# Kernel optimization log

Measured on AMD Instinct MI355X. Metric: run time of the kernel, lower is better.

The kernel has to match this reference:

```python
import jax, jax.numpy as jnp
import numpy as np

H = 3584          # hidden_size
NH = 28           # num query heads
NKV = 4           # num kv heads
HD = H // NH      # head_dim = 128
I = 18944         # intermediate_size
EPS = 1e-6
THETA = 1000000.0


def setup_inputs() -> dict:
    key = jax.random.key(0)
    ks = jax.random.split(key, 16)
    B, S = 1, 2048
    s = 0.02
    inp = {
        "hidden_states": jax.random.normal(ks[0], (B, S, H), jnp.float32),
        "position_ids": jnp.broadcast_to(jnp.arange(S, dtype=jnp.int32)[None, :], (B, S)),
        "q_w": jax.random.normal(ks[1], (NH * HD, H), jnp.float32) * s,
        "q_b": jax.random.normal(ks[2], (NH * HD,), jnp.float32) * s,
        "k_w": jax.random.normal(ks[3], (NKV * HD, H), jnp.float32) * s,
        "k_b": jax.random.normal(ks[4], (NKV * HD,), jnp.float32) * s,
        "v_w": jax.random.normal(ks[5], (NKV * HD, H), jnp.float32) * s,
        "v_b": jax.random.normal(ks[6], (NKV * HD,), jnp.float32) * s,
        "o_w": jax.random.normal(ks[7], (H, NH * HD), jnp.float32) * s,
        "gate_w": jax.random.normal(ks[8], (I, H), jnp.float32) * s,
        "up_w": jax.random.normal(ks[9], (I, H), jnp.float32) * s,
        "down_w": jax.random.normal(ks[10], (H, I), jnp.float32) * s,
        "ln1_w": jnp.ones((H,), jnp.float32),
        "ln2_w": jnp.ones((H,), jnp.float32),
    }
    return inp


def _rms_norm(x, w):
    var = jnp.mean(jnp.square(x), axis=-1, keepdims=True)
    return x * jax.lax.rsqrt(var + EPS) * w


def _rope_cos_sin(position_ids):
    # inv_freq: [HD/2]
    inv_freq = 1.0 / (THETA ** (jnp.arange(0, HD, 2, dtype=jnp.float32) / HD))
    ang = position_ids.astype(jnp.float32)[..., None] * inv_freq  # [B,S,HD/2]
    emb = jnp.concatenate([ang, ang], axis=-1)                     # [B,S,HD]
    return jnp.cos(emb)[:, None], jnp.sin(emb)[:, None]            # [B,1,S,HD]


def _rotate_half(x):
    x1, x2 = x[..., : HD // 2], x[..., HD // 2 :]
    return jnp.concatenate([-x2, x1], axis=-1)


def _forward(hidden_states, position_ids, q_w, q_b, k_w, k_b, v_w, v_b,
             o_w, gate_w, up_w, down_w, ln1_w, ln2_w):
    B, S, _ = hidden_states.shape
    residual = hidden_states
    x = _rms_norm(hidden_states, ln1_w)

    q = jnp.einsum("bsh,dh->bsd", x, q_w) + q_b   # [B,S,NH*HD]
    k = jnp.einsum("bsh,dh->bsd", x, k_w) + k_b   # [B,S,NKV*HD]
    v = jnp.einsum("bsh,dh->bsd", x, v_w) + v_b

    q = q.reshape(B, S, NH, HD).transpose(0, 2, 1, 3)    # [B,NH,S,HD]
    k = k.reshape(B, S, NKV, HD).transpose(0, 2, 1, 3)   # [B,NKV,S,HD]
    v = v.reshape(B, S, NKV, HD).transpose(0, 2, 1, 3)

    cos, sin = _rope_cos_sin(position_ids)
    q = q * cos + _rotate_half(q) * sin
    k = k * cos + _rotate_half(k) * sin

    # GQA: group query heads per kv head (NH = NKV * G)
    G = NH // NKV
    qg = q.reshape(B, NKV, G, S, HD)
    scores = jnp.einsum("bhgsd,bhtd->bhgst", qg, k) / jnp.sqrt(jnp.float32(HD))
    probs = jax.nn.softmax(scores, axis=-1)               # no causal mask in source
    attn = jnp.einsum("bhgst,bhtd->bhgsd", probs, v)      # [B,NKV,G,S,HD]
    attn = attn.reshape(B, NH, S, HD).transpose(0, 2, 1, 3).reshape(B, S, H)

    attn_out = jnp.einsum("bsd,hd->bsh", attn, o_w)
    hidden = residual + attn_out

    residual = hidden
    x = _rms_norm(hidden, ln2_w)
    gate = jax.nn.silu(jnp.einsum("bsh,ih->bsi", x, gate_w))
    up = jnp.einsum("bsh,ih->bsi", x, up_w)
    mlp = jnp.einsum("bsi,hi->bsh", gate * up, down_w)
    return residual + mlp


def reference(hidden_states, position_ids, q_w, q_b, k_w, k_b, v_w, v_b,
              o_w, gate_w, up_w, down_w, ln1_w, ln2_w):
    return _forward(hidden_states, position_ids, q_w, q_b, k_w, k_b, v_w, v_b,
                    o_w, gate_w, up_w, down_w, ln1_w, ln2_w)
```

## Files before the change

### kernel.cpp

```cpp
#include <hip/hip_runtime.h>
#include <hip/hip_bf16.h>
#include <stdint.h>

#define S_LEN 2048
#define HDIM  3584
#define NHEAD 28
#define NKVH  4
#define HDHD  128
#define IDIM  18944

typedef __attribute__((ext_vector_type(8))) short short8;
typedef __attribute__((ext_vector_type(4))) float floatx4;
typedef __attribute__((ext_vector_type(4))) unsigned int uint4v;

__device__ __forceinline__ unsigned short f2bf(float f) {
  union { float f; unsigned int u; } v; v.f = f;
  unsigned int r = v.u + 0x7fffu + ((v.u >> 16) & 1u);
  return (unsigned short)(r >> 16);
}
__device__ __forceinline__ float bf2f(unsigned short h) {
  union { unsigned int u; float f; } v; v.u = ((unsigned int)h) << 16;
  return v.f;
}
__device__ __forceinline__ unsigned int pk2(float a, float b) {
  __hip_bfloat162 h = __float22bfloat162_rn(make_float2(a, b));
  union { __hip_bfloat162 h; unsigned int u; } c; c.h = h; return c.u;
}

__device__ __forceinline__ void gload_lds16(const void* g, void* l) {
  __builtin_amdgcn_global_load_lds(
      (const __attribute__((address_space(1))) void*)g,
      (__attribute__((address_space(3))) void*)l, 16, 0, 0);
}

__device__ __forceinline__ int xcd_remap(int id, int total) {
  return (id & 7) * (total >> 3) + (id >> 3);
}

template<int BM, int MODE, bool BIAS>
__global__ __launch_bounds__(512, 2)
void gemm_db(const unsigned short* __restrict__ A, int lda,
             const unsigned short* __restrict__ W,
             const float* __restrict__ bias,
             void* __restrict__ outp, int ldo, int col0,
             const void* __restrict__ aux, int K)
{
  constexpr int MREP = BM / 32;
  constexpr int MSH  = (BM == 256) ? 3 : 4;
  constexpr int MT   = 2048 / BM;
  constexpr int APASS = BM / 64;

  const int g  = xcd_remap(blockIdx.x, gridDim.x);
  const int mb = g & (MT - 1);
  const int nb = g >> MSH;
  const int t  = threadIdx.x;
  const int w  = t >> 6, l = t & 63, lg = l >> 4, lc = l & 15;
  const int wr = w >> 2, wc = w & 3;

  __shared__ __align__(16) unsigned short As[2][BM * 64];
  __shared__ __align__(16) unsigned short Bs[2][256 * 64];

  floatx4 acc[MREP][4] = {};

  const char* Ablk = (const char*)(A + (size_t)mb * BM * lda);
  const char* Wblk = (const char*)(W + (size_t)nb * 256 * K);

  const int trow  = t >> 3;
  const int s_scb = (((t & 7) ^ ((t >> 3) & 7)) << 4);
  const int r_sw  = (lc & 7) << 4;

  const size_t abytes = (size_t)lda * 2;
  const size_t wbytes = (size_t)K * 2;

  auto stage = [&](int buf, int kt) {
    const char* asrc = Ablk + (size_t)kt * 128 + s_scb;
    #pragma unroll
    for (int i = 0; i < APASS; ++i)
      gload_lds16(asrc + (size_t)(i * 64 + trow) * abytes,
                  (char*)As[buf] + i * 8192 + t * 16);
    const char* wsrc = Wblk + (size_t)kt * 128 + s_scb;
    #pragma unroll
    for (int i = 0; i < 4; ++i)
      gload_lds16(wsrc + (size_t)(i * 64 + trow) * wbytes,
                  (char*)Bs[buf] + i * 8192 + t * 16);
  };

  const int nk = K >> 6;
  stage(0, 0);
  __syncthreads();

  int cur = 0;
  for (int kt = 0; kt < nk; ++kt) {
    if (kt + 1 < nk) stage(cur ^ 1, kt + 1);

    const char* ac = (const char*)As[cur];
    const char* bc = (const char*)Bs[cur];
    __builtin_amdgcn_s_setprio(1);
    #pragma unroll
    for (int kk = 0; kk < 2; ++kk) {
      const int ko = kk * 64 + lg * 16;
      short8 bfrag[4];
      #pragma unroll
      for (int n = 0; n < 4; ++n)
        bfrag[n] = *(const short8*)(bc + (wc*64 + n*16 + lc) * 128 + (ko ^ r_sw));
      #pragma unroll
      for (int m = 0; m < MREP; ++m) {
        short8 af = *(const short8*)(ac + (wr*(BM/2) + m*16 + lc) * 128 + (ko ^ r_sw));
        #pragma unroll
        for (int n = 0; n < 4; ++n)
          acc[m][n] = __builtin_amdgcn_mfma_f32_16x16x32_bf16(af, bfrag[n], acc[m][n], 0, 0, 0);
      }
    }
    __builtin_amdgcn_s_setprio(0);
    __syncthreads();
    cur ^= 1;
  }

  float bv[4] = {0.f, 0.f, 0.f, 0.f};
  if (BIAS) {
    #pragma unroll
    for (int n = 0; n < 4; ++n) bv[n] = bias[nb*256 + wc*64 + n*16 + lc];
  }
  #pragma unroll
  for (int m = 0; m < MREP; ++m) {
    #pragma unroll
    for (int n = 0; n < 4; ++n) {
      const int colg = col0 + nb*256 + wc*64 + n*16 + lc;
      #pragma unroll
      for (int j = 0; j < 4; ++j) {
        const int rowg = mb*BM + wr*(BM/2) + m*16 + lg*4 + j;
        const size_t oidx = (size_t)rowg * ldo + colg;
        float v = acc[m][n][j] + bv[n];
        if (MODE == 0) {
          ((float*)outp)[oidx] = v;
        } else if (MODE == 1) {
          ((unsigned short*)outp)[oidx] = f2bf(v);
        } else if (MODE == 2) {
          ((float*)outp)[oidx] = v + ((const float*)aux)[oidx];
        } else {
          float gt = bf2f(((const unsigned short*)aux)[oidx]);
          float sg = gt / (1.f + __expf(-gt));
          ((unsigned short*)outp)[oidx] = f2bf(sg * v);
        }
      }
    }
  }
}

__global__ __launch_bounds__(256)
void cvt_bf16_kernel(const float* __restrict__ in, unsigned short* __restrict__ out, int n8)
{
  int i = blockIdx.x * 256 + threadIdx.x;
  const int stride = gridDim.x * 256;
  for (; i < n8; i += stride) {
    floatx4 a = *(const floatx4*)(in + (size_t)i * 8);
    floatx4 b = *(const floatx4*)(in + (size_t)i * 8 + 4);
    uint4v p;
    p[0] = pk2(a[0], a[1]); p[1] = pk2(a[2], a[3]);
    p[2] = pk2(b[0], b[1]); p[3] = pk2(b[2], b[3]);
    *(uint4v*)(out + (size_t)i * 8) = p;
  }
}

__global__ void pack_bias_kernel(const float* __restrict__ qb, const float* __restrict__ kb,
                                 const float* __restrict__ vb, float* __restrict__ o)
{
  int i = blockIdx.x * 256 + threadIdx.x;
  if (i < 3584) o[i] = qb[i];
  else if (i < 4096) o[i] = kb[i - 3584];
  else if (i < 4608) o[i] = vb[i - 4096];
}

__global__ __launch_bounds__(448)
void rmsnorm_kernel(const float* __restrict__ x, const float* __restrict__ wgt,
                    unsigned short* __restrict__ out)
{
  const int row = blockIdx.x, t = threadIdx.x;
  const float* xp = x + (size_t)row * HDIM + t * 8;
  floatx4 a = *(const floatx4*)xp;
  floatx4 b = *(const floatx4*)(xp + 4);
  float ss = a[0]*a[0]+a[1]*a[1]+a[2]*a[2]+a[3]*a[3]
           + b[0]*b[0]+b[1]*b[1]+b[2]*b[2]+b[3]*b[3];
  #pragma unroll
  for (int mk = 1; mk < 64; mk <<= 1) ss += __shfl_xor(ss, mk, 64);
  __shared__ float wsum[8];
  if ((t & 63) == 0) wsum[t >> 6] = ss;
  __syncthreads();
  float tot = 0.f;
  #pragma unroll
  for (int i = 0; i < 7; ++i) tot += wsum[i];
  const float sc = rsqrtf(tot * (1.f / 3584.f) + 1e-6f);
  const float* wp = wgt + t * 8;
  short8 o;
  #pragma unroll
  for (int e = 0; e < 4; ++e) o[e]   = (short)f2bf(a[e] * sc * wp[e]);
  #pragma unroll
  for (int e = 0; e < 4; ++e) o[4+e] = (short)f2bf(b[e] * sc * wp[4+e]);
  *(short8*)(out + (size_t)row * HDIM + t * 8) = o;
}

__global__ __launch_bounds__(448)
void add_rmsnorm_kernel(const float* __restrict__ x, const float* __restrict__ y,
                        const float* __restrict__ wgt,
                        float* __restrict__ h1, unsigned short* __restrict__ out)
{
  const int row = blockIdx.x, t = threadIdx.x;
  const size_t base = (size_t)row * HDIM + t * 8;
  floatx4 a = *(const floatx4*)(x + base);
  floatx4 b = *(const floatx4*)(x + base + 4);
  floatx4 c = *(const floatx4*)(y + base);
  floatx4 d = *(const floatx4*)(y + base + 4);
  a += c; b += d;
  *(floatx4*)(h1 + base)     = a;
  *(floatx4*)(h1 + base + 4) = b;
  float ss = a[0]*a[0]+a[1]*a[1]+a[2]*a[2]+a[3]*a[3]
           + b[0]*b[0]+b[1]*b[1]+b[2]*b[2]+b[3]*b[3];
  #pragma unroll
  for (int mk = 1; mk < 64; mk <<= 1) ss += __shfl_xor(ss, mk, 64);
  __shared__ float wsum[8];
  if ((t & 63) == 0) wsum[t >> 6] = ss;
  __syncthreads();
  float tot = 0.f;
  #pragma unroll
  for (int i = 0; i < 7; ++i) tot += wsum[i];
  const float sc = rsqrtf(tot * (1.f / 3584.f) + 1e-6f);
  const float* wp = wgt + t * 8;
  short8 o;
  #pragma unroll
  for (int e = 0; e < 4; ++e) o[e]   = (short)f2bf(a[e] * sc * wp[e]);
  #pragma unroll
  for (int e = 0; e < 4; ++e) o[4+e] = (short)f2bf(b[e] * sc * wp[4+e]);
  *(short8*)(out + (size_t)row * HDIM + t * 8) = o;
}

__global__ void rope_table_kernel(const int* __restrict__ pos, float* __restrict__ tab)
{
  int idx = blockIdx.x * 256 + threadIdx.x;
  int s = idx >> 6, d = idx & 63;
  float p = (float)pos[s];
  float inv = expf(-((float)(2 * d) * (1.f / 128.f)) * 13.815510557964274f);
  float ang = p * inv;
  tab[idx] = cosf(ang);
  tab[S_LEN * 64 + idx] = sinf(ang);
}

template<int NHX>
__global__ void rope_apply_kernel(const float* __restrict__ in, const float* __restrict__ tab,
                                  unsigned short* __restrict__ out, int col0)
{
  int idx = blockIdx.x * 256 + threadIdx.x;
  int d = idx & 63;
  int rem = idx >> 6;
  int hh = rem % NHX;
  int s  = rem / NHX;
  const float* ip = in + (size_t)s * 4608 + col0 + hh * HDHD;
  float x1 = ip[d], x2 = ip[64 + d];
  float c  = tab[s * 64 + d];
  float sn = tab[S_LEN * 64 + s * 64 + d];
  unsigned short* op = out + (size_t)s * (NHX * HDHD) + hh * HDHD;
  op[d]      = f2bf(x1 * c - x2 * sn);
  op[64 + d] = f2bf(x2 * c + x1 * sn);
}

__global__ void vtrans_kernel(const float* __restrict__ qkvf, unsigned short* __restrict__ vt)
{
  int idx = blockIdx.x * 256 + threadIdx.x;
  int s = idx & (S_LEN - 1);
  int c = idx >> 11;
  vt[idx] = f2bf(qkvf[(size_t)s * 4608 + 4096 + c]);
}

__global__ __launch_bounds__(256)
void attn_kernel(const unsigned short* __restrict__ Q,
                 const unsigned short* __restrict__ Kr,
                 const unsigned short* __restrict__ Vt,
                 unsigned short* __restrict__ O)
{
  const int g  = xcd_remap(blockIdx.x, gridDim.x);
  const int qb = g & 31;
  const int h  = g >> 5;
  const int kvh = h / 7;
  const int t = threadIdx.x, w = t >> 6, l = t & 63, lg = l >> 4, lc = l & 15;

  __shared__ __align__(16) unsigned short Ks[64 * 128];
  __shared__ __align__(16) unsigned short Vs[128 * 64];
  __shared__ __align__(16) unsigned short Ps[4][16 * 64];

  const int qrow = qb * 64 + w * 16 + lc;
  short8 qf[4];
  {
    const unsigned short* qp = Q + (size_t)qrow * HDIM + h * HDHD + lg * 8;
    #pragma unroll
    for (int kk = 0; kk < 4; ++kk) qf[kk] = *(const short8*)(qp + kk * 32);
  }

  float mrun[4], lrun[4];
  #pragma unroll
  for (int j = 0; j < 4; ++j) { mrun[j] = -1e30f; lrun[j] = 0.f; }
  floatx4 oacc[8] = {};

  const int k_row = t >> 4;
  const int k_scb = (((t & 15) ^ ((t >> 4) & 7)) << 4);
  const int v_row = t >> 3;
  const int v_scb = (((t & 7) ^ ((t >> 3) & 7)) << 4);
  const int r_sw  = (lc & 7) << 4;
  const float scale = 0.08838834764831843f;

  for (int kt = 0; kt < 32; ++kt) {
    #pragma unroll
    for (int i = 0; i < 4; ++i)
      gload_lds16((const char*)Kr + ((size_t)(kt*64 + i*16 + k_row) * 512 + kvh*128) * 2 + k_scb,
                  (char*)Ks + i * 4096 + t * 16);
    #pragma unroll
    for (int i = 0; i < 4; ++i)
      gload_lds16((const char*)Vt + ((size_t)(kvh*128 + i*32 + v_row) * S_LEN) * 2
                      + (size_t)kt * 128 + v_scb,
                  (char*)Vs + i * 4096 + t * 16);
    __syncthreads();

    floatx4 sacc[4] = {};
    #pragma unroll
    for (int kk = 0; kk < 4; ++kk) {
      #pragma unroll
      for (int n = 0; n < 4; ++n) {
        short8 kf = *(const short8*)((const char*)Ks + (n*16 + lc) * 256
                                     + ((kk*64 + lg*16) ^ r_sw));
        sacc[n] = __builtin_amdgcn_mfma_f32_16x16x32_bf16(qf[kk], kf, sacc[n], 0, 0, 0);
      }
    }

    float pv[4][4], mt[4];
    #pragma unroll
    for (int j = 0; j < 4; ++j) {
      float a0 = sacc[0][j]*scale, a1 = sacc[1][j]*scale;
      float a2 = sacc[2][j]*scale, a3 = sacc[3][j]*scale;
      pv[0][j]=a0; pv[1][j]=a1; pv[2][j]=a2; pv[3][j]=a3;
      mt[j] = fmaxf(fmaxf(a0, a1), fmaxf(a2, a3));
    }
    #pragma unroll
    for (int mk = 1; mk < 16; mk <<= 1)
      #pragma unroll
      for (int j = 0; j < 4; ++j)
        mt[j] = fmaxf(mt[j], __shfl_xor(mt[j], mk, 16));

    float corr[4], rs[4];
    #pragma unroll
    for (int j = 0; j < 4; ++j) {
      float mn = fmaxf(mrun[j], mt[j]);
      corr[j] = __expf(mrun[j] - mn);
      mrun[j] = mn;
      rs[j] = 0.f;
    }
    #pragma unroll
    for (int n = 0; n < 4; ++n)
      #pragma unroll
      for (int j = 0; j < 4; ++j) {
        float p = __expf(pv[n][j] - mrun[j]);
        pv[n][j] = p; rs[j] += p;
      }
    #pragma unroll
    for (int mk = 1; mk < 16; mk <<= 1)
      #pragma unroll
      for (int j = 0; j < 4; ++j)
        rs[j] += __shfl_xor(rs[j], mk, 16);
    #pragma unroll
    for (int j = 0; j < 4; ++j) lrun[j] = lrun[j] * corr[j] + rs[j];
    #pragma unroll
    for (int q = 0; q < 8; ++q) {
      oacc[q][0] *= corr[0]; oacc[q][1] *= corr[1];
      oacc[q][2] *= corr[2]; oacc[q][3] *= corr[3];
    }

    char* pw = (char*)Ps[w];
    #pragma unroll
    for (int n = 0; n < 4; ++n)
      #pragma unroll
      for (int j = 0; j < 4; ++j) {
        const int prow = lg*4 + j;
        *(unsigned short*)(pw + prow*128 + ((((n*16 + lc)*2)) ^ ((prow & 7) << 4)))
            = f2bf(pv[n][j]);
      }

    short8 pa[2];
    #pragma unroll
    for (int ks = 0; ks < 2; ++ks)
      pa[ks] = *(const short8*)(pw + lc*128 + ((ks*64 + lg*16) ^ r_sw));
    #pragma unroll
    for (int ks = 0; ks < 2; ++ks)
      #pragma unroll
      for (int q = 0; q < 8; ++q) {
        short8 vf = *(const short8*)((const char*)Vs + (q*16 + lc) * 128
                                     + ((ks*64 + lg*16) ^ r_sw));
        oacc[q] = __builtin_amdgcn_mfma_f32_16x16x32_bf16(pa[ks], vf, oacc[q], 0, 0, 0);
      }
    __syncthreads();
  }

  float invl[4];
  #pragma unroll
  for (int j = 0; j < 4; ++j) invl[j] = 1.f / lrun[j];
  #pragma unroll
  for (int q = 0; q < 8; ++q)
    #pragma unroll
    for (int j = 0; j < 4; ++j) {
      int rowg = qb*64 + w*16 + lg*4 + j;
      int colg = h*HDHD + q*16 + lc;
      O[(size_t)rowg * HDIM + colg] = f2bf(oacc[q][j] * invl[j]);
    }
}

__global__ void sentinel_kernel(float* out, int n) {
  int i = blockIdx.x * 256 + threadIdx.x;
  if (i < n) out[i] = 1.0e6f;
}

extern "C" void kernel_launch(void* const* d_in, const int* in_sizes, int n_in,
                              void* d_out, int out_size, void* d_ws, size_t ws_size,
                              hipStream_t stream)
{
  (void)in_sizes; (void)n_in;
  const float* hidden = (const float*)d_in[0];
  const int*   pos    = (const int*)d_in[1];
  const float* q_w    = (const float*)d_in[2];
  const float* q_b    = (const float*)d_in[3];
  const float* k_w    = (const float*)d_in[4];
  const float* k_b    = (const float*)d_in[5];
  const float* v_w    = (const float*)d_in[6];
  const float* v_b    = (const float*)d_in[7];
  const float* o_w    = (const float*)d_in[8];
  const float* gate_w = (const float*)d_in[9];
  const float* up_w   = (const float*)d_in[10];
  const float* down_w = (const float*)d_in[11];
  const float* ln1    = (const float*)d_in[12];
  const float* ln2    = (const float*)d_in[13];
  float* out = (float*)d_out;
  char* ws = (char*)d_ws;

  unsigned short* XN    = (unsigned short*)(ws + 0);
  float*          QKVF  = (float*)(ws + 14680064);
  unsigned short* QR    = (unsigned short*)(ws + 52428800);
  unsigned short* KR    = (unsigned short*)(ws + 67108864);
  unsigned short* VT    = (unsigned short*)(ws + 69206016);
  float*          ROPET = (float*)(ws + 71303168);
  float*          BQKV  = (float*)(ws + 72351744);
  unsigned short* CTX   = (unsigned short*)(ws + 77594624);
  float*          AO    = (float*)(ws + 92274688);
  unsigned short* GBUF  = (unsigned short*)(ws + 0);
  unsigned short* ACT   = (unsigned short*)(ws + 77594624);
  float*          H1    = (float*)(ws + 155189248);
  unsigned short* XN2   = (unsigned short*)(ws + 184549376);
  unsigned short* WB    = (unsigned short*)(ws + 199229440);
  const size_t NEED_BIG = 199229440 + 135790592;

  if (ws_size < NEED_BIG) {
    sentinel_kernel<<<(out_size + 255) / 256, 256, 0, stream>>>(out, out_size);
    return;
  }

  const int CVG = 2048;

  rope_table_kernel<<<(S_LEN * 64) / 256, 256, 0, stream>>>(pos, ROPET);
  rmsnorm_kernel<<<S_LEN, 448, 0, stream>>>(hidden, ln1, XN);

  pack_bias_kernel<<<18, 256, 0, stream>>>(q_b, k_b, v_b, BQKV);
  cvt_bf16_kernel<<<CVG, 256, 0, stream>>>(q_w, WB,               (3584 * 3584) / 8);
  cvt_bf16_kernel<<<CVG, 256, 0, stream>>>(k_w, WB + 3584 * 3584, (512 * 3584) / 8);
  cvt_bf16_kernel<<<CVG, 256, 0, stream>>>(v_w, WB + 4096 * 3584, (512 * 3584) / 8);

  gemm_db<128, 0, true><<<288, 512, 0, stream>>>(XN, HDIM, WB, BQKV, QKVF, 4608, 0, nullptr, HDIM);

  rope_apply_kernel<28><<<(S_LEN * 28 * 64) / 256, 256, 0, stream>>>(QKVF, ROPET, QR, 0);
  rope_apply_kernel<4><<<(S_LEN * 4 * 64) / 256,  256, 0, stream>>>(QKVF, ROPET, KR, 3584);
  vtrans_kernel<<<(512 * S_LEN) / 256, 256, 0, stream>>>(QKVF, VT);

  cvt_bf16_kernel<<<CVG, 256, 0, stream>>>(o_w, WB, (3584 * 3584) / 8);

  attn_kernel<<<28 * 32, 256, 0, stream>>>(QR, KR, VT, CTX);

  gemm_db<128, 0, false><<<224, 512, 0, stream>>>(CTX, HDIM, WB, nullptr, AO, HDIM, 0, nullptr, HDIM);
  add_rmsnorm_kernel<<<S_LEN, 448, 0, stream>>>(hidden, AO, ln2, H1, XN2);

  cvt_bf16_kernel<<<CVG, 256, 0, stream>>>(gate_w, WB, (IDIM * HDIM) / 8);
  gemm_db<256, 1, false><<<592, 512, 0, stream>>>(XN2, HDIM, WB, nullptr, GBUF, IDIM, 0, nullptr, HDIM);

  cvt_bf16_kernel<<<CVG, 256, 0, stream>>>(up_w, WB, (IDIM * HDIM) / 8);
  gemm_db<256, 3, false><<<592, 512, 0, stream>>>(XN2, HDIM, WB, nullptr, ACT, IDIM, 0, GBUF, HDIM);

  cvt_bf16_kernel<<<CVG, 256, 0, stream>>>(down_w, WB, (HDIM * IDIM) / 8);
  gemm_db<128, 2, false><<<224, 512, 0, stream>>>(ACT, IDIM, WB, nullptr, out, HDIM, 0, H1, IDIM);
}
```

Measured before the change: 1.925 ms.

## Replace syncthreads with vmcnt-gated barriers and use 128-row tiles everywhere

The GEMM main loop now waits only for the previous stage's global-to-LDS loads with s_waitcnt vmcnt(6) and raw s_barrier. This lets the next tile's prefetch stay in flight across the barrier instead of draining all memory ops under __syncthreads. The gate/up GEMMs also switch from 256-row to 128-row M tiles, doubling the grid to 1184 blocks. That gives more parallelism but more weight re-reads and fewer MFMAs per B-fragment load.

```diff
diff --git a/kernel.cpp b/kernel.cpp
--- a/kernel.cpp
+++ b/kernel.cpp
@@ -37,83 +37,87 @@
   return (id & 7) * (total >> 3) + (id >> 3);
 }
 
-template<int BM, int MODE, bool BIAS>
+template<int MODE, bool BIAS>
 __global__ __launch_bounds__(512, 2)
-void gemm_db(const unsigned short* __restrict__ A, int lda,
-             const unsigned short* __restrict__ W,
-             const float* __restrict__ bias,
-             void* __restrict__ outp, int ldo, int col0,
-             const void* __restrict__ aux, int K)
-{
-  constexpr int MREP = BM / 32;
-  constexpr int MSH  = (BM == 256) ? 3 : 4;
-  constexpr int MT   = 2048 / BM;
-  constexpr int APASS = BM / 64;
-
+void gemm_p(const unsigned short* __restrict__ A, int lda,
+            const unsigned short* __restrict__ W,
+            const float* __restrict__ bias,
+            void* __restrict__ outp, int ldo, int col0,
+            const void* __restrict__ aux, int K)
+{
   const int g  = xcd_remap(blockIdx.x, gridDim.x);
-  const int mb = g & (MT - 1);
-  const int nb = g >> MSH;
+  const int mb = g & 15;
+  const int nb = g >> 4;
   const int t  = threadIdx.x;
   const int w  = t >> 6, l = t & 63, lg = l >> 4, lc = l & 15;
   const int wr = w >> 2, wc = w & 3;
 
-  __shared__ __align__(16) unsigned short As[2][BM * 64];
+  __shared__ __align__(16) unsigned short As[2][128 * 64];
   __shared__ __align__(16) unsigned short Bs[2][256 * 64];
 
-  floatx4 acc[MREP][4] = {};
-
-  const char* Ablk = (const char*)(A + (size_t)mb * BM * lda);
+  floatx4 acc[4][4] = {};
+
+  const char* Ablk = (const char*)(A + (size_t)mb * 128 * lda);
   const char* Wblk = (const char*)(W + (size_t)nb * 256 * K);
 
-  const int trow  = t >> 3;
-  const int s_scb = (((t & 7) ^ ((t >> 3) & 7)) << 4);
-  const int r_sw  = (lc & 7) << 4;
+  const int trow = t >> 3;
+  const int scb  = (((t & 7) ^ ((t >> 3) & 7)) << 4);
+  const int r_sw = (lc & 7) << 4;
 
   const size_t abytes = (size_t)lda * 2;
   const size_t wbytes = (size_t)K * 2;
 
   auto stage = [&](int buf, int kt) {
-    const char* asrc = Ablk + (size_t)kt * 128 + s_scb;
-    #pragma unroll
-    for (int i = 0; i < APASS; ++i)
-      gload_lds16(asrc + (size_t)(i * 64 + trow) * abytes,
+    const char* as = Ablk + (size_t)kt * 128 + scb;
+    #pragma unroll
+    for (int i = 0; i < 2; ++i)
+      gload_lds16(as + (size_t)(i * 64 + trow) * abytes,
                   (char*)As[buf] + i * 8192 + t * 16);
-    const char* wsrc = Wblk + (size_t)kt * 128 + s_scb;
+    const char* ws2 = Wblk + (size_t)kt * 128 + scb;
     #pragma unroll
     for (int i = 0; i < 4; ++i)
-      gload_lds16(wsrc + (size_t)(i * 64 + trow) * wbytes,
+      gload_lds16(ws2 + (size_t)(i * 64 + trow) * wbytes,
                   (char*)Bs[buf] + i * 8192 + t * 16);
   };
 
   const int nk = K >> 6;
   stage(0, 0);
-  __syncthreads();
-
-  int cur = 0;
+
   for (int kt = 0; kt < nk; ++kt) {
-    if (kt + 1 < nk) stage(cur ^ 1, kt + 1);
+    const int cur = kt & 1;
+    if (kt + 1 < nk) {
+      stage(cur ^ 1, kt + 1);
+      asm volatile("s_waitcnt vmcnt(6)" ::: "memory");
+    } else {
+      asm volatile("s_waitcnt vmcnt(0)" ::: "memory");
+    }
+    __builtin_amdgcn_sched_barrier(0);
+    __builtin_amdgcn_s_barrier();
+    __builtin_amdgcn_sched_barrier(0);
 
     const char* ac = (const char*)As[cur];
     const char* bc = (const char*)Bs[cur];
     __builtin_amdgcn_s_setprio(1);
     #pragma unroll
     for (int kk = 0; kk < 2; ++kk) {
-      const int ko = kk * 64 + lg * 16;
+      const int ko = (kk * 64 + lg * 16) ^ r_sw;
       short8 bfrag[4];
       #pragma unroll
       for (int n = 0; n < 4; ++n)
-        bfrag[n] = *(const short8*)(bc + (wc*64 + n*16 + lc) * 128 + (ko ^ r_sw));
-      #pragma unroll
-      for (int m = 0; m < MREP; ++m) {
-        short8 af = *(const short8*)(ac + (wr*(BM/2) + m*16 + lc) * 128 + (ko ^ r_sw));
+        bfrag[n] = *(const short8*)(bc + (wc * 64 + n * 16 + lc) * 128 + ko);
+      #pragma unroll
+      for (int m = 0; m < 4; ++m) {
+        short8 af = *(const short8*)(ac + (wr * 64 + m * 16 + lc) * 128 + ko);
         #pragma unroll
         for (int n = 0; n < 4; ++n)
           acc[m][n] = __builtin_amdgcn_mfma_f32_16x16x32_bf16(af, bfrag[n], acc[m][n], 0, 0, 0);
       }
     }
     __builtin_amdgcn_s_setprio(0);
-    __syncthreads();
-    cur ^= 1;
+    asm volatile("s_waitcnt lgkmcnt(0)" ::: "memory");
+    __builtin_amdgcn_sched_barrier(0);
+    __builtin_amdgcn_s_barrier();
+    __builtin_amdgcn_sched_barrier(0);
   }
 
   float bv[4] = {0.f, 0.f, 0.f, 0.f};
@@ -122,13 +126,13 @@
     for (int n = 0; n < 4; ++n) bv[n] = bias[nb*256 + wc*64 + n*16 + lc];
   }
   #pragma unroll
-  for (int m = 0; m < MREP; ++m) {
+  for (int m = 0; m < 4; ++m) {
     #pragma unroll
     for (int n = 0; n < 4; ++n) {
       const int colg = col0 + nb*256 + wc*64 + n*16 + lc;
       #pragma unroll
       for (int j = 0; j < 4; ++j) {
-        const int rowg = mb*BM + wr*(BM/2) + m*16 + lg*4 + j;
+        const int rowg = mb*128 + wr*64 + m*16 + lg*4 + j;
         const size_t oidx = (size_t)rowg * ldo + colg;
         float v = acc[m][n][j] + bv[n];
         if (MODE == 0) {
@@ -467,7 +471,7 @@
   cvt_bf16_kernel<<<CVG, 256, 0, stream>>>(k_w, WB + 3584 * 3584, (512 * 3584) / 8);
   cvt_bf16_kernel<<<CVG, 256, 0, stream>>>(v_w, WB + 4096 * 3584, (512 * 3584) / 8);
 
-  gemm_db<128, 0, true><<<288, 512, 0, stream>>>(XN, HDIM, WB, BQKV, QKVF, 4608, 0, nullptr, HDIM);
+  gemm_p<0, true><<<288, 512, 0, stream>>>(XN, HDIM, WB, BQKV, QKVF, 4608, 0, nullptr, HDIM);
 
   rope_apply_kernel<28><<<(S_LEN * 28 * 64) / 256, 256, 0, stream>>>(QKVF, ROPET, QR, 0);
   rope_apply_kernel<4><<<(S_LEN * 4 * 64) / 256,  256, 0, stream>>>(QKVF, ROPET, KR, 3584);
@@ -477,15 +481,15 @@
 
   attn_kernel<<<28 * 32, 256, 0, stream>>>(QR, KR, VT, CTX);
 
-  gemm_db<128, 0, false><<<224, 512, 0, stream>>>(CTX, HDIM, WB, nullptr, AO, HDIM, 0, nullptr, HDIM);
+  gemm_p<0, false><<<224, 512, 0, stream>>>(CTX, HDIM, WB, nullptr, AO, HDIM, 0, nullptr, HDIM);
   add_rmsnorm_kernel<<<S_LEN, 448, 0, stream>>>(hidden, AO, ln2, H1, XN2);
 
   cvt_bf16_kernel<<<CVG, 256, 0, stream>>>(gate_w, WB, (IDIM * HDIM) / 8);
-  gemm_db<256, 1, false><<<592, 512, 0, stream>>>(XN2, HDIM, WB, nullptr, GBUF, IDIM, 0, nullptr, HDIM);
+  gemm_p<1, false><<<1184, 512, 0, stream>>>(XN2, HDIM, WB, nullptr, GBUF, IDIM, 0, nullptr, HDIM);
 
   cvt_bf16_kernel<<<CVG, 256, 0, stream>>>(up_w, WB, (IDIM * HDIM) / 8);
-  gemm_db<256, 3, false><<<592, 512, 0, stream>>>(XN2, HDIM, WB, nullptr, ACT, IDIM, 0, GBUF, HDIM);
+  gemm_p<3, false><<<1184, 512, 0, stream>>>(XN2, HDIM, WB, nullptr, ACT, IDIM, 0, GBUF, HDIM);
 
   cvt_bf16_kernel<<<CVG, 256, 0, stream>>>(down_w, WB, (HDIM * IDIM) / 8);
-  gemm_db<128, 2, false><<<224, 512, 0, stream>>>(ACT, IDIM, WB, nullptr, out, HDIM, 0, H1, IDIM);
-}
+  gemm_p<2, false><<<224, 512, 0, stream>>>(ACT, IDIM, WB, nullptr, out, HDIM, 0, H1, IDIM);
+}
```

Result: slower. 2.068 ms (+7.4%).

## Replace double-buffered 512-thread GEMM with single-buffered 256x128-tile 4-wave GEMM

Applied to the files above, without the earlier changes.

All GEMMs now use one kernel with a fixed 256x128 output tile computed by 4 waves of 256 threads, and a single LDS stage instead of two. The aim is a smaller LDS footprint so more blocks can be resident per CU, with more, smaller blocks for the large MLP GEMMs. The cost is that global-to-LDS loads no longer overlap with MFMA work, the wave priority boost is dropped, and each block gets less weight reuse than the previous 256x256 tile. The epilogue store logic is moved into a shared helper.

```diff
diff --git a/kernel.cpp b/kernel.cpp
--- a/kernel.cpp
+++ b/kernel.cpp
@@ -37,111 +37,96 @@
   return (id & 7) * (total >> 3) + (id >> 3);
 }
 
-template<int BM, int MODE, bool BIAS>
-__global__ __launch_bounds__(512, 2)
-void gemm_db(const unsigned short* __restrict__ A, int lda,
-             const unsigned short* __restrict__ W,
-             const float* __restrict__ bias,
-             void* __restrict__ outp, int ldo, int col0,
-             const void* __restrict__ aux, int K)
-{
-  constexpr int MREP = BM / 32;
-  constexpr int MSH  = (BM == 256) ? 3 : 4;
-  constexpr int MT   = 2048 / BM;
-  constexpr int APASS = BM / 64;
-
+__device__ __forceinline__ void store_out(int MODE, void* outp, const void* aux,
+                                          size_t oidx, float v) {
+  if (MODE == 0) {
+    ((float*)outp)[oidx] = v;
+  } else if (MODE == 1) {
+    ((unsigned short*)outp)[oidx] = f2bf(v);
+  } else if (MODE == 2) {
+    ((float*)outp)[oidx] = v + ((const float*)aux)[oidx];
+  } else {
+    float gt = bf2f(((const unsigned short*)aux)[oidx]);
+    float sg = gt / (1.f + __expf(-gt));
+    ((unsigned short*)outp)[oidx] = f2bf(sg * v);
+  }
+}
+
+template<int MODE, bool BIAS>
+__global__ __launch_bounds__(256, 2)
+void gemm_w(const unsigned short* __restrict__ A, int lda,
+            const unsigned short* __restrict__ W,
+            const float* __restrict__ bias,
+            void* __restrict__ outp, int ldo, int col0,
+            const void* __restrict__ aux, int K)
+{
   const int g  = xcd_remap(blockIdx.x, gridDim.x);
-  const int mb = g & (MT - 1);
-  const int nb = g >> MSH;
+  const int mb = g & 7;
+  const int nb = g >> 3;
   const int t  = threadIdx.x;
   const int w  = t >> 6, l = t & 63, lg = l >> 4, lc = l & 15;
-  const int wr = w >> 2, wc = w & 3;
-
-  __shared__ __align__(16) unsigned short As[2][BM * 64];
-  __shared__ __align__(16) unsigned short Bs[2][256 * 64];
-
-  floatx4 acc[MREP][4] = {};
-
-  const char* Ablk = (const char*)(A + (size_t)mb * BM * lda);
-  const char* Wblk = (const char*)(W + (size_t)nb * 256 * K);
-
-  const int trow  = t >> 3;
+  const int wr = w >> 1, wc = w & 1;
+
+  __shared__ __align__(16) unsigned short As[256 * 64];
+  __shared__ __align__(16) unsigned short Bs[128 * 64];
+
+  floatx4 acc[8][4] = {};
+
+  const char* Ablk = (const char*)(A + (size_t)mb * 256 * lda);
+  const char* Wblk = (const char*)(W + (size_t)nb * 128 * K);
+
+  const int s_row = t >> 3;
   const int s_scb = (((t & 7) ^ ((t >> 3) & 7)) << 4);
   const int r_sw  = (lc & 7) << 4;
 
   const size_t abytes = (size_t)lda * 2;
   const size_t wbytes = (size_t)K * 2;
-
-  auto stage = [&](int buf, int kt) {
+  const int nk = K >> 6;
+
+  for (int kt = 0; kt < nk; ++kt) {
     const char* asrc = Ablk + (size_t)kt * 128 + s_scb;
     #pragma unroll
-    for (int i = 0; i < APASS; ++i)
-      gload_lds16(asrc + (size_t)(i * 64 + trow) * abytes,
-                  (char*)As[buf] + i * 8192 + t * 16);
+    for (int i = 0; i < 8; ++i)
+      gload_lds16(asrc + (size_t)(i * 32 + s_row) * abytes,
+                  (char*)As + i * 4096 + t * 16);
     const char* wsrc = Wblk + (size_t)kt * 128 + s_scb;
     #pragma unroll
     for (int i = 0; i < 4; ++i)
-      gload_lds16(wsrc + (size_t)(i * 64 + trow) * wbytes,
-                  (char*)Bs[buf] + i * 8192 + t * 16);
-  };
-
-  const int nk = K >> 6;
-  stage(0, 0);
-  __syncthreads();
-
-  int cur = 0;
-  for (int kt = 0; kt < nk; ++kt) {
-    if (kt + 1 < nk) stage(cur ^ 1, kt + 1);
-
-    const char* ac = (const char*)As[cur];
-    const char* bc = (const char*)Bs[cur];
-    __builtin_amdgcn_s_setprio(1);
+      gload_lds16(wsrc + (size_t)(i * 32 + s_row) * wbytes,
+                  (char*)Bs + i * 4096 + t * 16);
+    __syncthreads();
     #pragma unroll
     for (int kk = 0; kk < 2; ++kk) {
-      const int ko = kk * 64 + lg * 16;
-      short8 bfrag[4];
+      const int ko = (kk * 64 + lg * 16) ^ r_sw;
+      short8 bfr[4];
       #pragma unroll
       for (int n = 0; n < 4; ++n)
-        bfrag[n] = *(const short8*)(bc + (wc*64 + n*16 + lc) * 128 + (ko ^ r_sw));
-      #pragma unroll
-      for (int m = 0; m < MREP; ++m) {
-        short8 af = *(const short8*)(ac + (wr*(BM/2) + m*16 + lc) * 128 + (ko ^ r_sw));
+        bfr[n] = *(const short8*)((const char*)Bs + (wc*64 + n*16 + lc) * 128 + ko);
+      #pragma unroll
+      for (int m = 0; m < 8; ++m) {
+        short8 af = *(const short8*)((const char*)As + (wr*128 + m*16 + lc) * 128 + ko);
         #pragma unroll
         for (int n = 0; n < 4; ++n)
-          acc[m][n] = __builtin_amdgcn_mfma_f32_16x16x32_bf16(af, bfrag[n], acc[m][n], 0, 0, 0);
-      }
-    }
-    __builtin_amdgcn_s_setprio(0);
+          acc[m][n] = __builtin_amdgcn_mfma_f32_16x16x32_bf16(af, bfr[n], acc[m][n], 0, 0, 0);
+      }
+    }
     __syncthreads();
-    cur ^= 1;
   }
 
   float bv[4] = {0.f, 0.f, 0.f, 0.f};
   if (BIAS) {
     #pragma unroll
-    for (int n = 0; n < 4; ++n) bv[n] = bias[nb*256 + wc*64 + n*16 + lc];
-  }
-  #pragma unroll
-  for (int m = 0; m < MREP; ++m) {
+    for (int n = 0; n < 4; ++n) bv[n] = bias[nb*128 + wc*64 + n*16 + lc];
+  }
+  #pragma unroll
+  for (int m = 0; m < 8; ++m) {
     #pragma unroll
     for (int n = 0; n < 4; ++n) {
-      const int colg = col0 + nb*256 + wc*64 + n*16 + lc;
+      const int colg = col0 + nb*128 + wc*64 + n*16 + lc;
       #pragma unroll
       for (int j = 0; j < 4; ++j) {
-        const int rowg = mb*BM + wr*(BM/2) + m*16 + lg*4 + j;
-        const size_t oidx = (size_t)rowg * ldo + colg;
-        float v = acc[m][n][j] + bv[n];
-        if (MODE == 0) {
-          ((float*)outp)[oidx] = v;
-        } else if (MODE == 1) {
-          ((unsigned short*)outp)[oidx] = f2bf(v);
-        } else if (MODE == 2) {
-          ((float*)outp)[oidx] = v + ((const float*)aux)[oidx];
-        } else {
-          float gt = bf2f(((const unsigned short*)aux)[oidx]);
-          float sg = gt / (1.f + __expf(-gt));
-          ((unsigned short*)outp)[oidx] = f2bf(sg * v);
-        }
+        const int rowg = mb*256 + wr*128 + m*16 + lg*4 + j;
+        store_out(MODE, outp, aux, (size_t)rowg * ldo + colg, acc[m][n][j] + bv[n]);
       }
     }
   }
@@ -467,7 +452,7 @@
   cvt_bf16_kernel<<<CVG, 256, 0, stream>>>(k_w, WB + 3584 * 3584, (512 * 3584) / 8);
   cvt_bf16_kernel<<<CVG, 256, 0, stream>>>(v_w, WB + 4096 * 3584, (512 * 3584) / 8);
 
-  gemm_db<128, 0, true><<<288, 512, 0, stream>>>(XN, HDIM, WB, BQKV, QKVF, 4608, 0, nullptr, HDIM);
+  gemm_w<0, true><<<288, 256, 0, stream>>>(XN, HDIM, WB, BQKV, QKVF, 4608, 0, nullptr, HDIM);
 
   rope_apply_kernel<28><<<(S_LEN * 28 * 64) / 256, 256, 0, stream>>>(QKVF, ROPET, QR, 0);
   rope_apply_kernel<4><<<(S_LEN * 4 * 64) / 256,  256, 0, stream>>>(QKVF, ROPET, KR, 3584);
@@ -477,15 +462,15 @@
 
   attn_kernel<<<28 * 32, 256, 0, stream>>>(QR, KR, VT, CTX);
 
-  gemm_db<128, 0, false><<<224, 512, 0, stream>>>(CTX, HDIM, WB, nullptr, AO, HDIM, 0, nullptr, HDIM);
+  gemm_w<0, false><<<224, 256, 0, stream>>>(CTX, HDIM, WB, nullptr, AO, HDIM, 0, nullptr, HDIM);
   add_rmsnorm_kernel<<<S_LEN, 448, 0, stream>>>(hidden, AO, ln2, H1, XN2);
 
   cvt_bf16_kernel<<<CVG, 256, 0, stream>>>(gate_w, WB, (IDIM * HDIM) / 8);
-  gemm_db<256, 1, false><<<592, 512, 0, stream>>>(XN2, HDIM, WB, nullptr, GBUF, IDIM, 0, nullptr, HDIM);
+  gemm_w<1, false><<<1184, 256, 0, stream>>>(XN2, HDIM, WB, nullptr, GBUF, IDIM, 0, nullptr, HDIM);
 
   cvt_bf16_kernel<<<CVG, 256, 0, stream>>>(up_w, WB, (IDIM * HDIM) / 8);
-  gemm_db<256, 3, false><<<592, 512, 0, stream>>>(XN2, HDIM, WB, nullptr, ACT, IDIM, 0, GBUF, HDIM);
+  gemm_w<3, false><<<1184, 256, 0, stream>>>(XN2, HDIM, WB, nullptr, ACT, IDIM, 0, GBUF, HDIM);
 
   cvt_bf16_kernel<<<CVG, 256, 0, stream>>>(down_w, WB, (HDIM * IDIM) / 8);
-  gemm_db<128, 2, false><<<224, 512, 0, stream>>>(ACT, IDIM, WB, nullptr, out, HDIM, 0, H1, IDIM);
-}
+  gemm_w<2, false><<<224, 256, 0, stream>>>(ACT, IDIM, WB, nullptr, out, HDIM, 0, H1, IDIM);
+}
```

After: 1.782 ms. 7.4% less time.
